# Kernel optimization log

Measured on AMD Instinct MI355X. Metric: run time of the kernel, lower is better.

## Reference

```python
import jax, jax.numpy as jnp
import numpy as np

DT = 0.1
BOX = 1.0  # WORLD_SIZE
EPS = 1e-6


def range_angle(ang):
    return jnp.mod(ang + jnp.pi, 2.0 * jnp.pi) - jnp.pi


def ekf_step(x, P, a, Y, n1, n2_sigma, n2_kappa, gains, obs_gains):
    # x: (N,5) [px,py,ang,vel,ang_vel]; P: (N,5,5); a: (N,2); Y: (2,N)
    N = x.shape[0]
    dt = DT
    og = obs_gains

    # --- noise-free dynamics (w=0 in original forward) ---
    vel = gains[0] * a[:, 0]
    ang_vel = gains[1] * a[:, 1]
    ang = range_angle(x[:, 2] + ang_vel * dt)
    px = jnp.clip(x[:, 0] + vel * jnp.cos(ang) * dt, -BOX, BOX)
    py = jnp.clip(x[:, 1] + vel * jnp.sin(ang) * dt, -BOX, BOX)
    x_ = jnp.stack([px, py, ang, vel, ang_vel], axis=1)  # (N,5)

    # --- Jacobian A (N,5,5): eye(3) block + two trig entries ---
    d3 = jnp.arange(3)
    A = jnp.zeros((N, 5, 5), x.dtype)
    A = A.at[:, d3, d3].set(1.0)
    A = A.at[:, 0, 2].set(-vel * jnp.sin(ang) * dt)
    A = A.at[:, 1, 2].set(vel * jnp.cos(ang) * dt)

    # --- predict: L is identity in the original code, so L Q L^T = Q ---
    Q = jnp.diag(jnp.exp(2.0 * n1))
    P_ = jnp.einsum('nij,njk,nlk->nil', A, P, A) + Q  # (N,5,5)

    # --- innovation covariance S = H P_ H^T + M R M^T (R = I, M diag) ---
    # H = [0 | diag(og)] so H P_ H^T = diag(og) P_[3:5,3:5] diag(og)
    HPHt = P_[:, 3:5, 3:5] * og[None, :, None] * og[None, None, :]
    m_diag = x_[:, 3:5] ** 2 * jnp.exp(2.0 * n2_kappa) + jnp.exp(2.0 * n2_sigma)
    S = HPHt + m_diag[:, :, None] * jnp.eye(2, dtype=x.dtype)  # (N,2,2)

    # --- explicit 2x2 inverse ---
    sa, sb = S[:, 0, 0], S[:, 0, 1]
    sc, sd = S[:, 1, 0], S[:, 1, 1]
    det = sa * sd - sb * sc
    Sinv = jnp.stack([jnp.stack([sd, -sb], -1), jnp.stack([-sc, sa], -1)], -2)
    Sinv = Sinv / det[:, None, None]

    # --- Kalman gain K = P_ H^T S^{-1} ---
    PHt = P_[:, :, 3:5] * og[None, None, :]  # (N,5,2)
    K = jnp.einsum('nij,njk->nik', PHt, Sinv)  # (N,5,2)

    # --- update ---
    h = og[None, :] * x_[:, 3:5]  # noise-free observations (N,2)
    err = Y.T - h
    x_new = x_ + jnp.einsum('nij,nj->ni', K, err)

    KH = jnp.zeros((N, 5, 5), x.dtype).at[:, :, 3:5].set(K * og[None, None, :])
    I_KH = jnp.eye(5, dtype=x.dtype) - KH
    P_new = jnp.einsum('nij,njk->nik', I_KH, P_)
    P_new = 0.5 * (P_new + jnp.swapaxes(P_new, -1, -2)) + EPS * jnp.eye(5, dtype=x.dtype)
    return x_new, P_new, K


def setup_inputs() -> dict:
    key = jax.random.key(0)
    ks = jax.random.split(key, 6)
    N = 500_000
    x = jax.random.normal(ks[0], (N, 5), jnp.float32)
    # symmetric positive-definite covariances
    Lr = 0.1 * jax.random.normal(ks[1], (N, 5, 5), jnp.float32)
    P = jnp.einsum('nij,nkj->nik', Lr, Lr) + 0.5 * jnp.eye(5, dtype=jnp.float32)
    a = jax.random.normal(ks[2], (N, 2), jnp.float32)
    Y = 0.5 * jax.random.normal(ks[3], (2, N), jnp.float32)
    n1 = jnp.full((5,), -1.0, jnp.float32)
    n2 = jnp.full((4,), -1.0, jnp.float32)
    return {
        'x': x, 'P': P, 'a': a, 'Y': Y,
        'n1': n1,
        'n2_sigma': n2[:2],
        'n2_kappa': n2[2:],
        'gains': jnp.ones((2,), jnp.float32),
        'obs_gains': jnp.ones((2,), jnp.float32),
    }


def reference(x, P, a, Y, n1, n2_sigma, n2_kappa, gains, obs_gains):
    return ekf_step(x, P, a, Y, n1, n2_sigma, n2_kappa, gains, obs_gains)
```

## Files before the change

kernel.cpp:

```cpp
#include <hip/hip_runtime.h>
#include <math.h>
#include <stdint.h>


#define BLK 64

__device__ __forceinline__ void gload_lds16(const void* g, void* l) {
    __builtin_amdgcn_global_load_lds(
        (const __attribute__((address_space(1))) void*)g,
        (__attribute__((address_space(3))) void*)l, 16, 0, 0);
}
__device__ __forceinline__ void gload_lds4(const void* g, void* l) {
    __builtin_amdgcn_global_load_lds(
        (const __attribute__((address_space(1))) void*)g,
        (__attribute__((address_space(3))) void*)l, 4, 0, 0);
}

__global__ __launch_bounds__(BLK) void ekf_kernel(
    const float* __restrict__ xg,
    const float* __restrict__ Pg,
    const float* __restrict__ ag,
    const float* __restrict__ Yg,
    const float* __restrict__ n1,
    const float* __restrict__ n2s,
    const float* __restrict__ n2k,
    const float* __restrict__ gains,
    const float* __restrict__ og,
    float* __restrict__ out,
    int N)
{
    __shared__ float lds[BLK * 25 + BLK * 5 + BLK * 10];
    float* ldsP = lds;
    float* ldsX = lds + BLK * 25;
    float* ldsK = lds + BLK * 25 + BLK * 5;

    const int tid  = threadIdx.x;
    const int base = blockIdx.x * BLK;
    const int valid = min(BLK, N - base);
    if (valid <= 0) return;
    const bool full = (valid == BLK);

    if (full) {
        const char* gp = (const char*)(Pg + (size_t)base * 25);
        char* lp = (char*)ldsP;
        #pragma unroll
        for (int j = 0; j < 6; ++j)
            gload_lds16(gp + j * 1024 + tid * 16, lp + j * 1024);
        gload_lds4(gp + 6144 + tid * 4, lp + 6144);

        const char* gx = (const char*)(xg + (size_t)base * 5);
        char* lx = (char*)ldsX;
        gload_lds16(gx + tid * 16, lx);
        gload_lds4(gx + 1024 + tid * 4, lx + 1024);

        asm volatile("s_waitcnt vmcnt(0)" ::: "memory");
    } else {
        for (int k = tid; k < valid * 25; k += BLK) ldsP[k] = Pg[(size_t)base * 25 + k];
        for (int k = tid; k < valid * 5;  k += BLK) ldsX[k] = xg[(size_t)base * 5 + k];
    }
    __syncthreads();

    if (tid < valid) {
        const int i = base + tid;
        const float dt = 0.1f;
        const float fPI = 3.14159265358979323846f;
        const float f2PI = 6.28318530717958647692f;

        float2 ai = ((const float2*)ag)[i];
        float vel    = gains[0] * ai.x;
        float angvel = gains[1] * ai.y;

        float x0 = ldsX[tid * 5 + 0];
        float x1 = ldsX[tid * 5 + 1];
        float x2 = ldsX[tid * 5 + 2];

        float ar = x2 + angvel * dt + fPI;
        float w = fmodf(ar, f2PI);
        if (w < 0.0f) w += f2PI;
        float ang = w - fPI;

        float s, c;
        sincosf(ang, &s, &c);

        float px = fminf(fmaxf(x0 + vel * c * dt, -1.0f), 1.0f);
        float py = fminf(fmaxf(x1 + vel * s * dt, -1.0f), 1.0f);

        float m0 = -vel * s * dt;
        float m1 =  vel * c * dt;

        float p00 = ldsP[tid*25 + 0],  p01 = ldsP[tid*25 + 1],  p02 = ldsP[tid*25 + 2];
        float p10 = ldsP[tid*25 + 5],  p11 = ldsP[tid*25 + 6],  p12 = ldsP[tid*25 + 7];
        float p20 = ldsP[tid*25 + 10], p21 = ldsP[tid*25 + 11], p22 = ldsP[tid*25 + 12];

        float b00 = p00 + m0 * p20, b01 = p01 + m0 * p21, b02 = p02 + m0 * p22;
        float b10 = p10 + m1 * p20, b11 = p11 + m1 * p21, b12 = p12 + m1 * p22;
        float t00 = b00 + m0 * b02, t01 = b01 + m1 * b02, t02 = b02;
        float t10 = b10 + m0 * b12, t11 = b11 + m1 * b12, t12 = b12;
        float t20 = p20 + m0 * p22, t21 = p21 + m1 * p22, t22 = p22;

        float q0 = expf(2.0f * n1[0]);
        float q1 = expf(2.0f * n1[1]);
        float q2 = expf(2.0f * n1[2]);
        float q3 = expf(2.0f * n1[3]);
        float q4 = expf(2.0f * n1[4]);

        t00 += q0; t11 += q1; t22 += q2;

        const float EPS_ = 1e-6f;
        float s01 = 0.5f * (t01 + t10);
        float s02 = 0.5f * (t02 + t20);
        float s12 = 0.5f * (t12 + t21);
        t00 += EPS_; t11 += EPS_; t22 += EPS_;

        float og0 = og[0], og1 = og[1];
        float e2s0 = expf(2.0f * n2s[0]), e2s1 = expf(2.0f * n2s[1]);
        float e2k0 = expf(2.0f * n2k[0]), e2k1 = expf(2.0f * n2k[1]);

        float S00 = q3 * og0 * og0 + vel * vel * e2k0 + e2s0;
        float S11 = q4 * og1 * og1 + angvel * angvel * e2k1 + e2s1;

        float K30 = q3 * og0 / S00;
        float K41 = q4 * og1 / S11;

        float y0 = Yg[i], y1 = Yg[N + i];
        float err0 = y0 - og0 * vel;
        float err1 = y1 - og1 * angvel;

        float xn3 = vel    + K30 * err0;
        float xn4 = angvel + K41 * err1;

        float g3 = 1.0f - K30 * og0;
        float g4 = 1.0f - K41 * og1;
        float Pn33 = g3 * q3 + EPS_;
        float Pn44 = g4 * q4 + EPS_;

        ldsX[tid*5 + 0] = px;
        ldsX[tid*5 + 1] = py;
        ldsX[tid*5 + 2] = ang;
        ldsX[tid*5 + 3] = xn3;
        ldsX[tid*5 + 4] = xn4;

        float* pp = ldsP + tid * 25;
        pp[0]  = t00;  pp[1]  = s01;  pp[2]  = s02;  pp[3]  = 0.0f; pp[4]  = 0.0f;
        pp[5]  = s01;  pp[6]  = t11;  pp[7]  = s12;  pp[8]  = 0.0f; pp[9]  = 0.0f;
        pp[10] = s02;  pp[11] = s12;  pp[12] = t22;  pp[13] = 0.0f; pp[14] = 0.0f;
        pp[15] = 0.0f; pp[16] = 0.0f; pp[17] = 0.0f; pp[18] = Pn33; pp[19] = 0.0f;
        pp[20] = 0.0f; pp[21] = 0.0f; pp[22] = 0.0f; pp[23] = 0.0f; pp[24] = Pn44;

        float* kk = ldsK + tid * 10;
        kk[0] = 0.0f; kk[1] = 0.0f; kk[2] = 0.0f; kk[3] = 0.0f;
        kk[4] = 0.0f; kk[5] = 0.0f;
        kk[6] = K30;  kk[7] = 0.0f;
        kk[8] = 0.0f; kk[9] = K41;
    }
    __syncthreads();

    float* gx = out + (size_t)base * 5;
    float* gp = out + (size_t)5 * N + (size_t)base * 25;
    float* gk = out + (size_t)30 * N + (size_t)base * 10;

    if (full) {
        float4* gx4 = (float4*)gx;  const float4* lx4 = (const float4*)ldsX;
        float4* gp4 = (float4*)gp;  const float4* lp4 = (const float4*)ldsP;
        float4* gk4 = (float4*)gk;  const float4* lk4 = (const float4*)ldsK;

        gx4[tid] = lx4[tid];
        if (tid < 16) gx4[64 + tid] = lx4[64 + tid];
        #pragma unroll
        for (int j = 0; j < 6; ++j) gp4[j * 64 + tid] = lp4[j * 64 + tid];
        if (tid < 16) gp4[384 + tid] = lp4[384 + tid];
        #pragma unroll
        for (int j = 0; j < 2; ++j) gk4[j * 64 + tid] = lk4[j * 64 + tid];
        if (tid < 32) gk4[128 + tid] = lk4[128 + tid];
    } else {
        for (int k = tid; k < valid * 5;  k += BLK) gx[k] = ldsX[k];
        for (int k = tid; k < valid * 25; k += BLK) gp[k] = ldsP[k];
        for (int k = tid; k < valid * 10; k += BLK) gk[k] = ldsK[k];
    }
}

extern "C" void kernel_launch(void* const* d_in, const int* in_sizes, int n_in,
                              void* d_out, int out_size, void* d_ws, size_t ws_size,
                              hipStream_t stream) {
    const float* x     = (const float*)d_in[0];
    const float* P     = (const float*)d_in[1];
    const float* a     = (const float*)d_in[2];
    const float* Y     = (const float*)d_in[3];
    const float* n1    = (const float*)d_in[4];
    const float* n2s   = (const float*)d_in[5];
    const float* n2k   = (const float*)d_in[6];
    const float* gains = (const float*)d_in[7];
    const float* og    = (const float*)d_in[8];
    const int N = in_sizes[0] / 5;
    const int grid = (N + BLK - 1) / BLK;
    ekf_kernel<<<grid, BLK, 0, stream>>>(x, P, a, Y, n1, n2s, n2k, gains, og,
                                         (float*)d_out, N);
}
```

Measured before the change: 153.1 us.

## Use persistent blocks with double-buffered async LDS prefetch of next tile

Replaces one-block-per-tile launch with a fixed grid of 1280 persistent 64-thread blocks that each process a contiguous range of tiles. The next tile's P, x, a and Y are prefetched into a second LDS buffer with global_load_lds while the current tile is computed, using vmcnt waits in place of barriers. Per-block constants (exps, gains) are hoisted out of the loop and the constant zero entries of the output staging buffer are written once. This aims to hide load latency and cut launch/setup overhead, but with single-wave blocks and no barriers it depends on wave-level LDS ordering and hand-counted vmcnt values, and a grid of 1280 one-wave blocks may leave the device with less occupancy.

```diff
diff --git a/kernel.cpp b/kernel.cpp
--- a/kernel.cpp
+++ b/kernel.cpp
@@ -4,6 +4,13 @@
 
 
 #define BLK 64
+#define TILE_F 2176
+#define OFF_X  1600
+#define OFF_A  1920
+#define OFF_Y  2048
+#define OB_X   0
+#define OB_P   320
+#define OB_K   1920
 
 __device__ __forceinline__ void gload_lds16(const void* g, void* l) {
     __builtin_amdgcn_global_load_lds(
@@ -16,166 +23,212 @@
         (__attribute__((address_space(3))) void*)l, 4, 0, 0);
 }
 
+__device__ __forceinline__ void stage_tile(const float* Pg, const float* xg,
+                                           const float* ag, const float* Yg,
+                                           int N, int base, float* buf, int tid) {
+    const char* gp = (const char*)(Pg + (size_t)base * 25);
+    char* lp = (char*)buf;
+    #pragma unroll
+    for (int j = 0; j < 6; ++j)
+        gload_lds16(gp + j * 1024 + tid * 16, lp + j * 1024);
+    gload_lds4(gp + 6144 + tid * 4, lp + 6144);
+    const char* gx = (const char*)(xg + (size_t)base * 5);
+    gload_lds16(gx + tid * 16, lp + 6400);
+    gload_lds4(gx + 1024 + tid * 4, lp + 6400 + 1024);
+    const char* ga = (const char*)(ag + (size_t)base * 2);
+    gload_lds4(ga + tid * 4,       lp + 7680);
+    gload_lds4(ga + 256 + tid * 4, lp + 7680 + 256);
+    gload_lds4((const char*)(Yg + base)     + tid * 4, lp + 8192);
+    gload_lds4((const char*)(Yg + N + base) + tid * 4, lp + 8192 + 256);
+}
+
+struct EkfOut {
+    float px, py, ang, xn3, xn4;
+    float t00, s01, s02, t11, s12, t22, Pn33, Pn44;
+    float K30, K41;
+};
+
+__device__ __forceinline__ EkfOut ekf_math(
+    float x0, float x1, float x2, float a0, float a1, float y0, float y1,
+    float p00, float p01, float p02, float p10, float p11, float p12,
+    float p20, float p21, float p22,
+    float g0, float g1, float og0, float og1,
+    float q0, float q1, float q2, float q3, float q4,
+    float e2s0, float e2s1, float e2k0, float e2k1)
+{
+    const float dt = 0.1f;
+    const float fPI  = 3.14159265358979323846f;
+    const float f2PI = 6.28318530717958647692f;
+    const float EPS_ = 1e-6f;
+
+    float vel = g0 * a0, angvel = g1 * a1;
+
+    float ar = x2 + angvel * dt + fPI;
+    float w = fmodf(ar, f2PI);
+    if (w < 0.0f) w += f2PI;
+    float ang = w - fPI;
+
+    float s, c;
+    sincosf(ang, &s, &c);
+
+    EkfOut o;
+    o.px = fminf(fmaxf(x0 + vel * c * dt, -1.0f), 1.0f);
+    o.py = fminf(fmaxf(x1 + vel * s * dt, -1.0f), 1.0f);
+    o.ang = ang;
+
+    float m0 = -vel * s * dt, m1 = vel * c * dt;
+
+    float b00 = p00 + m0 * p20, b01 = p01 + m0 * p21, b02 = p02 + m0 * p22;
+    float b10 = p10 + m1 * p20, b11 = p11 + m1 * p21, b12 = p12 + m1 * p22;
+    float t00 = b00 + m0 * b02, t01 = b01 + m1 * b02;
+    float t10 = b10 + m0 * b12, t11 = b11 + m1 * b12;
+    float t20 = p20 + m0 * p22, t21 = p21 + m1 * p22, t22 = p22;
+    float t02 = b02, t12 = b12;
+
+    t00 += q0; t11 += q1; t22 += q2;
+    o.s01 = 0.5f * (t01 + t10);
+    o.s02 = 0.5f * (t02 + t20);
+    o.s12 = 0.5f * (t12 + t21);
+    o.t00 = t00 + EPS_; o.t11 = t11 + EPS_; o.t22 = t22 + EPS_;
+
+    float S00 = q3 * og0 * og0 + vel * vel * e2k0 + e2s0;
+    float S11 = q4 * og1 * og1 + angvel * angvel * e2k1 + e2s1;
+    o.K30 = q3 * og0 / S00;
+    o.K41 = q4 * og1 / S11;
+
+    o.xn3 = vel    + o.K30 * (y0 - og0 * vel);
+    o.xn4 = angvel + o.K41 * (y1 - og1 * angvel);
+    o.Pn33 = (1.0f - o.K30 * og0) * q3 + EPS_;
+    o.Pn44 = (1.0f - o.K41 * og1) * q4 + EPS_;
+    return o;
+}
+
 __global__ __launch_bounds__(BLK) void ekf_kernel(
-    const float* __restrict__ xg,
-    const float* __restrict__ Pg,
-    const float* __restrict__ ag,
-    const float* __restrict__ Yg,
-    const float* __restrict__ n1,
-    const float* __restrict__ n2s,
-    const float* __restrict__ n2k,
-    const float* __restrict__ gains,
-    const float* __restrict__ og,
-    float* __restrict__ out,
-    int N)
+    const float* __restrict__ xg, const float* __restrict__ Pg,
+    const float* __restrict__ ag, const float* __restrict__ Yg,
+    const float* __restrict__ n1, const float* __restrict__ n2s,
+    const float* __restrict__ n2k, const float* __restrict__ gains,
+    const float* __restrict__ og, float* __restrict__ out, int N)
 {
-    __shared__ float lds[BLK * 25 + BLK * 5 + BLK * 10];
-    float* ldsP = lds;
-    float* ldsX = lds + BLK * 25;
-    float* ldsK = lds + BLK * 25 + BLK * 5;
-
-    const int tid  = threadIdx.x;
-    const int base = blockIdx.x * BLK;
-    const int valid = min(BLK, N - base);
-    if (valid <= 0) return;
-    const bool full = (valid == BLK);
-
-    if (full) {
-        const char* gp = (const char*)(Pg + (size_t)base * 25);
-        char* lp = (char*)ldsP;
-        #pragma unroll
-        for (int j = 0; j < 6; ++j)
-            gload_lds16(gp + j * 1024 + tid * 16, lp + j * 1024);
-        gload_lds4(gp + 6144 + tid * 4, lp + 6144);
-
-        const char* gx = (const char*)(xg + (size_t)base * 5);
-        char* lx = (char*)ldsX;
-        gload_lds16(gx + tid * 16, lx);
-        gload_lds4(gx + 1024 + tid * 4, lx + 1024);
-
-        asm volatile("s_waitcnt vmcnt(0)" ::: "memory");
-    } else {
-        for (int k = tid; k < valid * 25; k += BLK) ldsP[k] = Pg[(size_t)base * 25 + k];
-        for (int k = tid; k < valid * 5;  k += BLK) ldsX[k] = xg[(size_t)base * 5 + k];
+    __shared__ float lds[2 * TILE_F + 2560];
+    float* bufA = lds;
+    float* bufB = lds + TILE_F;
+    float* obuf = lds + 2 * TILE_F;
+
+    const int tid = threadIdx.x;
+    const int tiles = (N + BLK - 1) / BLK;
+    const int G = gridDim.x, b = blockIdx.x;
+    const int q = tiles / G, r = tiles % G;
+    const int t0 = b * q + min(b, r);
+    const int myTiles = q + (b < r ? 1 : 0);
+    if (myTiles <= 0) return;
+
+    const float g0 = gains[0], g1 = gains[1];
+    const float og0 = og[0], og1 = og[1];
+    const float q0 = expf(2.f * n1[0]), q1 = expf(2.f * n1[1]),
+                q2 = expf(2.f * n1[2]), q3 = expf(2.f * n1[3]),
+                q4 = expf(2.f * n1[4]);
+    const float e2s0 = expf(2.f * n2s[0]), e2s1 = expf(2.f * n2s[1]);
+    const float e2k0 = expf(2.f * n2k[0]), e2k1 = expf(2.f * n2k[1]);
+
+    {
+        float* pp = obuf + OB_P + tid * 25;
+        pp[3] = 0.f; pp[4] = 0.f; pp[8] = 0.f; pp[9] = 0.f;
+        pp[13] = 0.f; pp[14] = 0.f;
+        pp[15] = 0.f; pp[16] = 0.f; pp[17] = 0.f; pp[19] = 0.f;
+        pp[20] = 0.f; pp[21] = 0.f; pp[22] = 0.f; pp[23] = 0.f;
+        float* kk = obuf + OB_K + tid * 10;
+        kk[0] = 0.f; kk[1] = 0.f; kk[2] = 0.f; kk[3] = 0.f;
+        kk[4] = 0.f; kk[5] = 0.f; kk[7] = 0.f; kk[8] = 0.f;
     }
-    __syncthreads();
-
-    if (tid < valid) {
-        const int i = base + tid;
-        const float dt = 0.1f;
-        const float fPI = 3.14159265358979323846f;
-        const float f2PI = 6.28318530717958647692f;
-
-        float2 ai = ((const float2*)ag)[i];
-        float vel    = gains[0] * ai.x;
-        float angvel = gains[1] * ai.y;
-
-        float x0 = ldsX[tid * 5 + 0];
-        float x1 = ldsX[tid * 5 + 1];
-        float x2 = ldsX[tid * 5 + 2];
-
-        float ar = x2 + angvel * dt + fPI;
-        float w = fmodf(ar, f2PI);
-        if (w < 0.0f) w += f2PI;
-        float ang = w - fPI;
-
-        float s, c;
-        sincosf(ang, &s, &c);
-
-        float px = fminf(fmaxf(x0 + vel * c * dt, -1.0f), 1.0f);
-        float py = fminf(fmaxf(x1 + vel * s * dt, -1.0f), 1.0f);
-
-        float m0 = -vel * s * dt;
-        float m1 =  vel * c * dt;
-
-        float p00 = ldsP[tid*25 + 0],  p01 = ldsP[tid*25 + 1],  p02 = ldsP[tid*25 + 2];
-        float p10 = ldsP[tid*25 + 5],  p11 = ldsP[tid*25 + 6],  p12 = ldsP[tid*25 + 7];
-        float p20 = ldsP[tid*25 + 10], p21 = ldsP[tid*25 + 11], p22 = ldsP[tid*25 + 12];
-
-        float b00 = p00 + m0 * p20, b01 = p01 + m0 * p21, b02 = p02 + m0 * p22;
-        float b10 = p10 + m1 * p20, b11 = p11 + m1 * p21, b12 = p12 + m1 * p22;
-        float t00 = b00 + m0 * b02, t01 = b01 + m1 * b02, t02 = b02;
-        float t10 = b10 + m0 * b12, t11 = b11 + m1 * b12, t12 = b12;
-        float t20 = p20 + m0 * p22, t21 = p21 + m1 * p22, t22 = p22;
-
-        float q0 = expf(2.0f * n1[0]);
-        float q1 = expf(2.0f * n1[1]);
-        float q2 = expf(2.0f * n1[2]);
-        float q3 = expf(2.0f * n1[3]);
-        float q4 = expf(2.0f * n1[4]);
-
-        t00 += q0; t11 += q1; t22 += q2;
-
-        const float EPS_ = 1e-6f;
-        float s01 = 0.5f * (t01 + t10);
-        float s02 = 0.5f * (t02 + t20);
-        float s12 = 0.5f * (t12 + t21);
-        t00 += EPS_; t11 += EPS_; t22 += EPS_;
-
-        float og0 = og[0], og1 = og[1];
-        float e2s0 = expf(2.0f * n2s[0]), e2s1 = expf(2.0f * n2s[1]);
-        float e2k0 = expf(2.0f * n2k[0]), e2k1 = expf(2.0f * n2k[1]);
-
-        float S00 = q3 * og0 * og0 + vel * vel * e2k0 + e2s0;
-        float S11 = q4 * og1 * og1 + angvel * angvel * e2k1 + e2s1;
-
-        float K30 = q3 * og0 / S00;
-        float K41 = q4 * og1 / S11;
-
-        float y0 = Yg[i], y1 = Yg[N + i];
-        float err0 = y0 - og0 * vel;
-        float err1 = y1 - og1 * angvel;
-
-        float xn3 = vel    + K30 * err0;
-        float xn4 = angvel + K41 * err1;
-
-        float g3 = 1.0f - K30 * og0;
-        float g4 = 1.0f - K41 * og1;
-        float Pn33 = g3 * q3 + EPS_;
-        float Pn44 = g4 * q4 + EPS_;
-
-        ldsX[tid*5 + 0] = px;
-        ldsX[tid*5 + 1] = py;
-        ldsX[tid*5 + 2] = ang;
-        ldsX[tid*5 + 3] = xn3;
-        ldsX[tid*5 + 4] = xn4;
-
-        float* pp = ldsP + tid * 25;
-        pp[0]  = t00;  pp[1]  = s01;  pp[2]  = s02;  pp[3]  = 0.0f; pp[4]  = 0.0f;
-        pp[5]  = s01;  pp[6]  = t11;  pp[7]  = s12;  pp[8]  = 0.0f; pp[9]  = 0.0f;
-        pp[10] = s02;  pp[11] = s12;  pp[12] = t22;  pp[13] = 0.0f; pp[14] = 0.0f;
-        pp[15] = 0.0f; pp[16] = 0.0f; pp[17] = 0.0f; pp[18] = Pn33; pp[19] = 0.0f;
-        pp[20] = 0.0f; pp[21] = 0.0f; pp[22] = 0.0f; pp[23] = 0.0f; pp[24] = Pn44;
-
-        float* kk = ldsK + tid * 10;
-        kk[0] = 0.0f; kk[1] = 0.0f; kk[2] = 0.0f; kk[3] = 0.0f;
-        kk[4] = 0.0f; kk[5] = 0.0f;
-        kk[6] = K30;  kk[7] = 0.0f;
-        kk[8] = 0.0f; kk[9] = K41;
+
+    {
+        int base0 = t0 * BLK;
+        if (base0 + BLK <= N) stage_tile(Pg, xg, ag, Yg, N, base0, bufA, tid);
     }
-    __syncthreads();
-
-    float* gx = out + (size_t)base * 5;
-    float* gp = out + (size_t)5 * N + (size_t)base * 25;
-    float* gk = out + (size_t)30 * N + (size_t)base * 10;
-
-    if (full) {
-        float4* gx4 = (float4*)gx;  const float4* lx4 = (const float4*)ldsX;
-        float4* gp4 = (float4*)gp;  const float4* lp4 = (const float4*)ldsP;
-        float4* gk4 = (float4*)gk;  const float4* lk4 = (const float4*)ldsK;
-
-        gx4[tid] = lx4[tid];
-        if (tid < 16) gx4[64 + tid] = lx4[64 + tid];
-        #pragma unroll
-        for (int j = 0; j < 6; ++j) gp4[j * 64 + tid] = lp4[j * 64 + tid];
-        if (tid < 16) gp4[384 + tid] = lp4[384 + tid];
-        #pragma unroll
-        for (int j = 0; j < 2; ++j) gk4[j * 64 + tid] = lk4[j * 64 + tid];
-        if (tid < 32) gk4[128 + tid] = lk4[128 + tid];
-    } else {
-        for (int k = tid; k < valid * 5;  k += BLK) gx[k] = ldsX[k];
-        for (int k = tid; k < valid * 25; k += BLK) gp[k] = ldsP[k];
-        for (int k = tid; k < valid * 10; k += BLK) gk[k] = ldsK[k];
+    float* cur = bufA;
+    float* nxt = bufB;
+
+    for (int k = 0; k < myTiles; ++k) {
+        const int t = t0 + k;
+        const int base = t * BLK;
+        const bool fullT = (base + BLK <= N);
+
+        bool issued = false;
+        if (k + 1 < myTiles) {
+            int nb = (t + 1) * BLK;
+            if (nb + BLK <= N) { stage_tile(Pg, xg, ag, Yg, N, nb, nxt, tid); issued = true; }
+        }
+
+        if (fullT) {
+            if (k == 0) { if (issued) asm volatile("s_waitcnt vmcnt(13)" ::: "memory");
+                          else        asm volatile("s_waitcnt vmcnt(0)"  ::: "memory"); }
+            else        { if (issued) asm volatile("s_waitcnt vmcnt(25)" ::: "memory");
+                          else        asm volatile("s_waitcnt vmcnt(12)" ::: "memory"); }
+
+            float x0 = cur[OFF_X + tid * 5 + 0];
+            float x1 = cur[OFF_X + tid * 5 + 1];
+            float x2 = cur[OFF_X + tid * 5 + 2];
+            float2 av = *(const float2*)&cur[OFF_A + tid * 2];
+            float y0 = cur[OFF_Y + tid];
+            float y1 = cur[OFF_Y + 64 + tid];
+            const float* pr = cur + tid * 25;
+            EkfOut o = ekf_math(x0, x1, x2, av.x, av.y, y0, y1,
+                                pr[0], pr[1], pr[2], pr[5], pr[6], pr[7],
+                                pr[10], pr[11], pr[12],
+                                g0, g1, og0, og1, q0, q1, q2, q3, q4,
+                                e2s0, e2s1, e2k0, e2k1);
+
+            float* xx = obuf + OB_X + tid * 5;
+            xx[0] = o.px; xx[1] = o.py; xx[2] = o.ang; xx[3] = o.xn3; xx[4] = o.xn4;
+            float* pp = obuf + OB_P + tid * 25;
+            pp[0] = o.t00; pp[1] = o.s01; pp[2] = o.s02;
+            pp[5] = o.s01; pp[6] = o.t11; pp[7] = o.s12;
+            pp[10] = o.s02; pp[11] = o.s12; pp[12] = o.t22;
+            pp[18] = o.Pn33; pp[24] = o.Pn44;
+            float* kk = obuf + OB_K + tid * 10;
+            kk[6] = o.K30; kk[9] = o.K41;
+
+            float4* gx4 = (float4*)(out + (size_t)base * 5);
+            float4* gp4 = (float4*)(out + (size_t)5 * N + (size_t)base * 25);
+            float4* gk4 = (float4*)(out + (size_t)30 * N + (size_t)base * 10);
+            const float4* lx4 = (const float4*)(obuf + OB_X);
+            const float4* lp4 = (const float4*)(obuf + OB_P);
+            const float4* lk4 = (const float4*)(obuf + OB_K);
+            gx4[tid] = lx4[tid];
+            if (tid < 16) gx4[64 + tid] = lx4[64 + tid];
+            #pragma unroll
+            for (int j = 0; j < 6; ++j) gp4[j * 64 + tid] = lp4[j * 64 + tid];
+            if (tid < 16) gp4[384 + tid] = lp4[384 + tid];
+            #pragma unroll
+            for (int j = 0; j < 2; ++j) gk4[j * 64 + tid] = lk4[j * 64 + tid];
+            if (tid < 32) gk4[128 + tid] = lk4[128 + tid];
+        } else {
+            const int i = base + tid;
+            if (i < N) {
+                const float* pr = Pg + (size_t)i * 25;
+                EkfOut o = ekf_math(xg[i * 5 + 0], xg[i * 5 + 1], xg[i * 5 + 2],
+                                    ag[i * 2 + 0], ag[i * 2 + 1],
+                                    Yg[i], Yg[N + i],
+                                    pr[0], pr[1], pr[2], pr[5], pr[6], pr[7],
+                                    pr[10], pr[11], pr[12],
+                                    g0, g1, og0, og1, q0, q1, q2, q3, q4,
+                                    e2s0, e2s1, e2k0, e2k1);
+                float* gx = out + (size_t)i * 5;
+                gx[0] = o.px; gx[1] = o.py; gx[2] = o.ang; gx[3] = o.xn3; gx[4] = o.xn4;
+                float* gp = out + (size_t)5 * N + (size_t)i * 25;
+                gp[0] = o.t00; gp[1] = o.s01; gp[2] = o.s02; gp[3] = 0.f; gp[4] = 0.f;
+                gp[5] = o.s01; gp[6] = o.t11; gp[7] = o.s12; gp[8] = 0.f; gp[9] = 0.f;
+                gp[10] = o.s02; gp[11] = o.s12; gp[12] = o.t22; gp[13] = 0.f; gp[14] = 0.f;
+                gp[15] = 0.f; gp[16] = 0.f; gp[17] = 0.f; gp[18] = o.Pn33; gp[19] = 0.f;
+                gp[20] = 0.f; gp[21] = 0.f; gp[22] = 0.f; gp[23] = 0.f; gp[24] = o.Pn44;
+                float* gk = out + (size_t)30 * N + (size_t)i * 10;
+                gk[0] = 0.f; gk[1] = 0.f; gk[2] = 0.f; gk[3] = 0.f; gk[4] = 0.f;
+                gk[5] = 0.f; gk[6] = o.K30; gk[7] = 0.f; gk[8] = 0.f; gk[9] = o.K41;
+            }
+        }
+
+        float* tmp = cur; cur = nxt; nxt = tmp;
     }
 }
 
@@ -192,7 +245,9 @@
     const float* gains = (const float*)d_in[7];
     const float* og    = (const float*)d_in[8];
     const int N = in_sizes[0] / 5;
-    const int grid = (N + BLK - 1) / BLK;
-    ekf_kernel<<<grid, BLK, 0, stream>>>(x, P, a, Y, n1, n2s, n2k, gains, og,
-                                         (float*)d_out, N);
-}
+    const int tiles = (N + BLK - 1) / BLK;
+    int G = 1280;
+    if (G > tiles) G = tiles;
+    ekf_kernel<<<G, BLK, 0, stream>>>(x, P, a, Y, n1, n2s, n2k, gains, og,
+                                      (float*)d_out, N);
+}
```

After: 150.1 us. 1.02x faster.
